# Optimization experiments

Hardware: AMD Instinct MI355X
Metric: run time of the kernel (lower is better)

## Reference

```python
import jax, jax.numpy as jnp
import numpy as np

GEN_POLY = ("1011011", "1111001")  # constraint_length 7, rate 1/2
LARGE = 1e9  # metric for infeasible start states


def _build_trellis(gen_poly):
    """Static trellis tables (numpy, built at trace time).

    State = last mu input bits (most recent bit is MSB), matching the
    shift-register convention: next_state = [u, s_bits[:-1]].
    """
    conv_n = len(gen_poly)
    K = len(gen_poly[0])
    mu = K - 1
    ns, ni, no = 2 ** mu, 2, 2 ** conv_n
    g = np.array([[int(c) for c in p] for p in gen_poly])  # (conv_n, K)
    to_nodes = np.zeros((ns, ni), np.int32)
    op = np.zeros((ns, ni), np.int32)
    for s in range(ns):
        s_bits = [(s >> (mu - 1 - i)) & 1 for i in range(mu)]
        for u in range(ni):
            reg = np.array([u] + s_bits)          # [u_t, u_{t-1}, ..., u_{t-mu}]
            outs = (g @ reg) % 2                  # conv_n output bits
            op[s, u] = int("".join(map(str, outs)), 2)
            to_nodes[s, u] = int("".join(map(str, [u] + s_bits[:-1])), 2)
    from_nodes = np.zeros((ns, ni), np.int32)
    op_by_tonode = np.zeros((ns, ni), np.int32)
    cnt = np.zeros(ns, np.int32)
    for s in range(ns):
        for u in range(ni):
            t = to_nodes[s, u]
            from_nodes[t, cnt[t]] = s
            op_by_tonode[t, cnt[t]] = op[s, u]
            cnt[t] += 1
    op_bits = np.array([[(o >> (conv_n - 1 - j)) & 1 for j in range(conv_n)]
                        for o in range(no)], np.float32)  # (no, conv_n)
    return conv_n, ns, ni, to_nodes, from_nodes, op_by_tonode, op_bits


def setup_inputs() -> dict:
    key = jax.random.key(0)
    # noisy channel LLRs for B=512 codewords of length n=4096
    inputs = jax.random.normal(key, (512, 4096), dtype=jnp.float32) * 2.0
    return {"inputs": inputs}


def reference(inputs):
    conv_n, ns, ni, to_nodes_np, from_nodes_np, op_by_tonode_np, op_bits = \
        _build_trellis(GEN_POLY)
    tn = jnp.asarray(to_nodes_np)       # (ns, ni) next state
    fn = jnp.asarray(from_nodes_np)     # (ns, ni) predecessor states
    opt = jnp.asarray(op_by_tonode_np)  # (ns, ni) output symbol on that branch

    B, n = inputs.shape
    T = n // conv_n                     # number of trellis steps / info bits
    y = inputs.reshape(B, T, conv_n)

    # soft_llr branch metrics: bm[t,b,o] = sum_c y[b,t,c] * (1 - 2*op_bit[o,c])
    sign = jnp.asarray(1.0 - 2.0 * op_bits)          # (no, conv_n)
    bm = jnp.einsum('btc,oc->tbo', y, sign)          # (T, B, no)

    cum0 = jnp.full((B, ns), LARGE, jnp.float32).at[:, 0].set(0.0)
    st_rng = jnp.arange(ns)

    def acs(cum, bm_t):
        # add: metric of (prev_state i, output symbol j)
        sm = bm_t[:, None, :] + cum[:, :, None]      # (B, ns, no)
        # gather by to-node: candidates for each next state
        cand = sm[:, fn, opt]                        # (B, ns, ni)
        j = jnp.argmin(cand, axis=2)                 # compare-select
        tb = fn[st_rng[None, :], j]                  # traceback predecessor (B, ns)
        cum_t = jnp.min(cand, axis=2)
        return cum_t, (cum_t, tb)

    cum_T, (cms, tbs) = jax.lax.scan(acs, cum0, bm)  # tbs: (T, B, ns)

    # traceback from optimal terminal state
    term = jnp.argmin(cum_T, axis=1).astype(jnp.int32)

    def tb_step(st, tb_t):
        prev = jnp.take_along_axis(tb_t, st[:, None], axis=1)[:, 0]
        return prev, st

    p0, ys = jax.lax.scan(tb_step, term, tbs[1:], reverse=True)
    # path states at times 0..T (initial state is 0)
    paths = jnp.concatenate(
        [jnp.zeros((B, 1), jnp.int32), p0[:, None], jnp.swapaxes(ys, 0, 1)],
        axis=1)                                       # (B, T+1)

    # recover input bit per transition: bit u s.t. to_nodes[prev, u] == next
    match = tn[paths[:, :-1]] == paths[:, 1:][:, :, None]  # (B, T, ni)
    bits = jnp.sum(jnp.where(match, jnp.arange(ni, dtype=jnp.int32), 0), axis=-1)
    return bits.astype(jnp.float32)                   # (B, T) hard bit estimates
```

## Files before the change

### kernel.cpp

```cpp
#include <hip/hip_runtime.h>
#include <stdint.h>

#define T_STEPS 2048
#define NCHUNK  86
#define LARGEF  1.0e9f
#define NB      512
typedef unsigned long long u64;
typedef unsigned uint2v __attribute__((ext_vector_type(2)));

__device__ __forceinline__ int par6(int x) { return __builtin_popcount((unsigned)x) & 1; }

constexpr int CARR[6] = {5, 6, 12, 8, 16, 32};

template<int CTRL>
__device__ __forceinline__ float xdpp(float x) {
  return __int_as_float(__builtin_amdgcn_update_dpp(0, __float_as_int(x), CTRL, 0xF, 0xF, true));
}
template<int CTRL>
__device__ __forceinline__ unsigned xdpp_u(unsigned x) {
  return (unsigned)__builtin_amdgcn_update_dpp(0, (int)x, CTRL, 0xF, 0xF, true);
}
__device__ __forceinline__ unsigned selmask_u(unsigned a_false, unsigned b_true, u64 m) {
  unsigned out;
  asm("v_cndmask_b32 %0, %1, %2, %3" : "=v"(out) : "v"(a_false), "v"(b_true), "s"(m));
  return out;
}
__device__ __forceinline__ unsigned exch16_u(unsigned x, u64 mrx) {
#if __has_builtin(__builtin_amdgcn_permlane16_swap)
  uint2v r = __builtin_amdgcn_permlane16_swap(x, x, false, false);
  return selmask_u(r.y, r.x, mrx);
#else
  (void)mrx;
  return (unsigned)__builtin_amdgcn_ds_swizzle((int)x, 0x401F);
#endif
}
__device__ __forceinline__ unsigned exch32_u(unsigned x, u64 mrx) {
#if __has_builtin(__builtin_amdgcn_permlane32_swap)
  uint2v r = __builtin_amdgcn_permlane32_swap(x, x, false, false);
  return selmask_u(r.y, r.x, mrx);
#else
  (void)mrx;
  return (unsigned)__shfl_xor((int)x, 32, 64);
#endif
}
template<int PH>
__device__ __forceinline__ float exchf(float x, const u64 (&mrx)[2]) {
  if constexpr (PH == 0) return xdpp<0xB1>(x);
  else if constexpr (PH == 1) return xdpp<0x4E>(x);
  else if constexpr (PH == 2) return xdpp<0x141>(x);
  else if constexpr (PH == 3) return xdpp<0x140>(x);
  else if constexpr (PH == 4) return __uint_as_float(exch16_u(__float_as_uint(x), mrx[0]));
  else return __uint_as_float(exch32_u(__float_as_uint(x), mrx[1]));
}
template<int PH>
__device__ __forceinline__ unsigned exchu(unsigned x, const u64 (&mrx)[2]) {
  if constexpr (PH == 0) return xdpp_u<0xB1>(x);
  else if constexpr (PH == 1) return xdpp_u<0x4E>(x);
  else if constexpr (PH == 2) return xdpp_u<0x141>(x);
  else if constexpr (PH == 3) return xdpp_u<0x140>(x);
  else if constexpr (PH == 4) return exch16_u(x, mrx[0]);
  else return exch32_u(x, mrx[1]);
}

struct Phc {
  float sae[6], sbe[6];
  unsigned sgn[6];
  unsigned pdu[6];
  u64 pdm[6];
  u64 mrx[2];
};

__device__ __forceinline__ void mkconsts(int lane, Phc& p) {
#pragma unroll
  for (int ph = 0; ph < 6; ++ph) {
    const int pdv = par6(lane & CARR[ph]);
    int t = 0;
#pragma unroll
    for (int j = 0; j < 5; ++j) t |= par6(lane & CARR[(ph + 1 + j) % 6]) << j;
    t |= pdv << 5;
    const float sa = 1.0f - 2.0f * (float)par6(t & 45);
    const float sb = 1.0f - 2.0f * (float)par6(t & 60);
    p.sae[ph] = pdv ? -sa : sa;
    p.sbe[ph] = pdv ? -sb : sb;
    p.sgn[ph] = pdv ? 0u : 0x80000000u;
    p.pdu[ph] = (unsigned)pdv;
    p.pdm[ph] = __ballot(pdv != 0);
  }
  const u64 ODD16 = 0xFFFF0000FFFF0000ull, HI32 = 0xFFFFFFFF00000000ull;
#if __has_builtin(__builtin_amdgcn_permlane16_swap)
  {
    uint2v r = __builtin_amdgcn_permlane16_swap((unsigned)lane, (unsigned)lane, false, false);
    p.mrx[0] = (((unsigned)__builtin_amdgcn_readlane((int)r.x, 0) == 16u)) ? ~ODD16 : ODD16;
  }
#else
  p.mrx[0] = 0;
#endif
#if __has_builtin(__builtin_amdgcn_permlane32_swap)
  {
    uint2v r = __builtin_amdgcn_permlane32_swap((unsigned)lane, (unsigned)lane, false, false);
    p.mrx[1] = (((unsigned)__builtin_amdgcn_readlane((int)r.x, 0) == 32u)) ? ~HI32 : HI32;
  }
#else
  p.mrx[1] = 0;
#endif
}

template<int N>
__device__ __forceinline__ void bmcalc(const float4 (&fy)[12], float (&bm)[24],
                                       const float (&sae)[6], const float (&sbe)[6]) {
#pragma unroll
  for (int k = 0; k < N; ++k) {
    const int ph = k % 6;
    const float y0 = (k & 1) ? fy[k >> 1].z : fy[k >> 1].x;
    const float y1 = (k & 1) ? fy[k >> 1].w : fy[k >> 1].y;
    bm[k] = fmaf(sae[ph], y0, sbe[ph] * y1);
  }
}

template<int N, int K>
__device__ __forceinline__ void acs(float& cum, unsigned& dw, const float (&bm)[24],
                                    const unsigned (&sgn)[6], const u64 (&mrx)[2]) {
  if constexpr (K < N) {
    constexpr int ph = K % 6;
    const float ex = exchf<ph>(cum, mrx);
    const float cA = cum + bm[K];
    const float cB = ex - bm[K];
    const float D = cA - cB;
    cum = fminf(cA, cB);
    unsigned tmp;
    asm("v_xor_b32 %0, %2, %3\n\t"
        "v_cmp_gt_f32 vcc, 0, %0\n\t"
        "v_addc_co_u32 %1, vcc, %1, %1, vcc"
        : "=&v"(tmp), "+v"(dw)
        : "v"(D), "v"(sgn[ph]) : "vcc");
    acs<N, K + 1>(cum, dw, bm, sgn, mrx);
  }
}

template<int N, int K>
__device__ __forceinline__ void wrec(unsigned& word, unsigned& dws, const unsigned (&pdu)[6],
                                     const u64 (&pdm)[6], const u64 (&mrx)[2]) {
  if constexpr (K < N) {
    constexpr int ph = K % 6;
    const unsigned exw = exchu<ph>(word, mrx);
    asm("v_cmp_gt_i32 vcc, 0, %1\n\t"
        "v_add_u32 %1, %1, %1\n\t"
        "s_xor_b64 vcc, vcc, %3\n\t"
        "v_cndmask_b32 %0, %0, %2, vcc"
        : "+v"(word), "+v"(dws)
        : "v"(exw), "s"(pdm[ph]) : "vcc");
    word |= pdu[ph] << (6 + K);
    wrec<N, K + 1>(word, dws, pdu, pdm, mrx);
  }
}

__device__ __forceinline__ int term_argmin(float cum, int lane) {
  const int stf = par6(lane & 12) | (par6(lane & 8) << 1) | (par6(lane & 16) << 2) |
                  (par6(lane & 32) << 3) | (par6(lane & 5) << 4) | (par6(lane & 6) << 5);
  float v = cum; int bs = stf; int bl = lane;
#pragma unroll
  for (int off = 32; off >= 1; off >>= 1) {
    const float ov = __shfl_xor(v, off, 64);
    const int os = __shfl_xor(bs, off, 64);
    const int ol = __shfl_xor(bl, off, 64);
    if (ov < v || (ov == v && os < bs)) { v = ov; bs = os; bl = ol; }
  }
  return bl;
}

__global__ __launch_bounds__(64, 1) void vit_fwd(const float* __restrict__ in,
                                                 unsigned* __restrict__ dwg,
                                                 int* __restrict__ term) {
  __shared__ float y_lds[2 * T_STEPS];
  const int b = blockIdx.x;
  const int lane = threadIdx.x;
  {
    const float4* g = (const float4*)(in + (size_t)b * (2 * T_STEPS));
    float4* l = (float4*)y_lds;
#pragma unroll
    for (int i = 0; i < 16; ++i) l[i * 64 + lane] = g[i * 64 + lane];
  }
  __syncthreads();

  Phc p;
  mkconsts(lane, p);

  float cum = (lane == 0) ? 0.0f : LARGEF;
  float bm[24];
  float4 cur[12], nxt[12];
  const float4* y4 = (const float4*)y_lds;
  unsigned* dwp = dwg + (size_t)b * (NCHUNK * 64) + lane;
  unsigned dw;
#pragma unroll
  for (int j = 0; j < 12; ++j) cur[j] = y4[j];
  for (int cc = 0; cc < 42; ++cc) {
    const int c0 = 2 * cc;
    bmcalc<24>(cur, bm, p.sae, p.sbe);
#pragma unroll
    for (int j = 0; j < 12; ++j) nxt[j] = y4[12 * (c0 + 1) + j];
    dw = 0; acs<24, 0>(cum, dw, bm, p.sgn, p.mrx);
    *dwp = dw; dwp += 64;
    bmcalc<24>(nxt, bm, p.sae, p.sbe);
#pragma unroll
    for (int j = 0; j < 12; ++j) cur[j] = y4[12 * (c0 + 2) + j];
    dw = 0; acs<24, 0>(cum, dw, bm, p.sgn, p.mrx);
    *dwp = dw; dwp += 64;
  }
  bmcalc<24>(cur, bm, p.sae, p.sbe);
#pragma unroll
  for (int j = 0; j < 4; ++j) nxt[j] = y4[1020 + j];
  dw = 0; acs<24, 0>(cum, dw, bm, p.sgn, p.mrx);
  *dwp = dw; dwp += 64;
  bmcalc<8>(nxt, bm, p.sae, p.sbe);
  dw = 0; acs<8, 0>(cum, dw, bm, p.sgn, p.mrx);
  *dwp = dw;

  const int bl = term_argmin(cum, lane);
  if (lane == 0) term[b] = bl;
}

__global__ __launch_bounds__(256, 1) void vit_rec(const unsigned* __restrict__ dwg,
                                                  unsigned* __restrict__ tbfg) {
  const int tid = threadIdx.x;
  const int lane = tid & 63;
  const int wv = tid >> 6;
  const int idx = blockIdx.x * 4 + wv;
  const unsigned ui = (unsigned)idx;
  const int c = (int)(ui % (unsigned)NCHUNK);

  Phc p;
  mkconsts(lane, p);

  const unsigned dw = dwg[(size_t)idx * 64 + lane];
  unsigned word = (unsigned)lane;
  if (c == NCHUNK - 1) {
    unsigned dws = dw << 24;
    wrec<8, 0>(word, dws, p.pdu, p.pdm, p.mrx);
  } else {
    unsigned dws = dw << 8;
    wrec<24, 0>(word, dws, p.pdu, p.pdm, p.mrx);
  }
  tbfg[(size_t)idx * 64 + lane] = word;
}

__global__ __launch_bounds__(64, 1) void vit_tb(const unsigned* __restrict__ tbfg,
                                                const int* __restrict__ term,
                                                float* __restrict__ out) {
  const int b = blockIdx.x;
  const int lane = threadIdx.x;
  unsigned rows[NCHUNK];
  const unsigned* tp = tbfg + (size_t)b * (NCHUNK * 64) + lane;
#pragma unroll
  for (int c = 0; c < NCHUNK; ++c) rows[c] = tp[c * 64];
  int lam = term[b];
  const size_t ob = (size_t)b * T_STEPS;
#pragma unroll
  for (int cc = 0; cc < NCHUNK; ++cc) {
    const int c = NCHUNK - 1 - cc;
    const unsigned w = (unsigned)__builtin_amdgcn_readlane((int)rows[c], lam);
    const int nb = (c == NCHUNK - 1) ? 8 : 24;
    if (lane < nb) out[ob + c * 24 + lane] = (float)((w >> (6 + lane)) & 1u);
    lam = (int)(w & 63u);
  }
}

__global__ __launch_bounds__(64, 1) void vit_fb(const float* __restrict__ in,
                                                float* __restrict__ out) {
  __shared__ float y_lds[2 * T_STEPS];
  __shared__ unsigned dwl[NCHUNK][64];
  __shared__ unsigned tbf[NCHUNK][64];
  const int b = blockIdx.x;
  const int lane = threadIdx.x;
  {
    const float4* g = (const float4*)(in + (size_t)b * (2 * T_STEPS));
    float4* l = (float4*)y_lds;
#pragma unroll
    for (int i = 0; i < 16; ++i) l[i * 64 + lane] = g[i * 64 + lane];
  }
  __syncthreads();
  Phc p;
  mkconsts(lane, p);
  float cum = (lane == 0) ? 0.0f : LARGEF;
  float bm[24];
  float4 cur[12], nxt[12];
  const float4* y4 = (const float4*)y_lds;
  unsigned dw;
#pragma unroll
  for (int j = 0; j < 12; ++j) cur[j] = y4[j];
  for (int cc = 0; cc < 42; ++cc) {
    const int c0 = 2 * cc;
    bmcalc<24>(cur, bm, p.sae, p.sbe);
#pragma unroll
    for (int j = 0; j < 12; ++j) nxt[j] = y4[12 * (c0 + 1) + j];
    dw = 0; acs<24, 0>(cum, dw, bm, p.sgn, p.mrx);
    dwl[c0][lane] = dw;
    bmcalc<24>(nxt, bm, p.sae, p.sbe);
#pragma unroll
    for (int j = 0; j < 12; ++j) cur[j] = y4[12 * (c0 + 2) + j];
    dw = 0; acs<24, 0>(cum, dw, bm, p.sgn, p.mrx);
    dwl[c0 + 1][lane] = dw;
  }
  bmcalc<24>(cur, bm, p.sae, p.sbe);
#pragma unroll
  for (int j = 0; j < 4; ++j) nxt[j] = y4[1020 + j];
  dw = 0; acs<24, 0>(cum, dw, bm, p.sgn, p.mrx);
  dwl[84][lane] = dw;
  bmcalc<8>(nxt, bm, p.sae, p.sbe);
  dw = 0; acs<8, 0>(cum, dw, bm, p.sgn, p.mrx);
  dwl[85][lane] = dw;

  for (int c = 0; c < 85; ++c) {
    unsigned dws = dwl[c][lane] << 8;
    unsigned word = (unsigned)lane;
    wrec<24, 0>(word, dws, p.pdu, p.pdm, p.mrx);
    tbf[c][lane] = word;
  }
  {
    unsigned dws = dwl[85][lane] << 24;
    unsigned word = (unsigned)lane;
    wrec<8, 0>(word, dws, p.pdu, p.pdm, p.mrx);
    tbf[85][lane] = word;
  }

  int lam = __builtin_amdgcn_readfirstlane(term_argmin(cum, lane));
  const size_t ob = (size_t)b * T_STEPS;
  unsigned row = tbf[85][lane];
  for (int c = 85; c >= 0; --c) {
    unsigned nrow = 0;
    if (c > 0) nrow = tbf[c - 1][lane];
    const unsigned w = (unsigned)__builtin_amdgcn_readlane((int)row, lam);
    const int nb = (c == 85) ? 8 : 24;
    if (lane < nb) out[ob + c * 24 + lane] = (float)((w >> (6 + lane)) & 1u);
    lam = (int)(w & 63u);
    row = nrow;
  }
}

extern "C" void kernel_launch(void* const* d_in, const int* in_sizes, int n_in,
                              void* d_out, int out_size, void* d_ws, size_t ws_size,
                              hipStream_t stream) {
  const float* in = (const float*)d_in[0];
  float* out = (float*)d_out;
  (void)in_sizes; (void)n_in; (void)out_size;
  const size_t nwords = (size_t)NB * NCHUNK * 64;
  const size_t need = nwords * 4 * 2 + NB * 4;
  if (ws_size >= need) {
    unsigned* dwg = (unsigned*)d_ws;
    unsigned* tbfg = dwg + nwords;
    int* term = (int*)(tbfg + nwords);
    vit_fwd<<<dim3(NB), dim3(64), 0, stream>>>(in, dwg, term);
    vit_rec<<<dim3((NB * NCHUNK) / 4), dim3(256), 0, stream>>>(dwg, tbfg);
    vit_tb<<<dim3(NB), dim3(64), 0, stream>>>(tbfg, term, out);
  } else {
    vit_fb<<<dim3(NB), dim3(64), 0, stream>>>(in, out);
  }
}
```

Baseline: 75.94 us.

## Checkpoint path metrics in forward pass and recompute decisions per chunk in parallel

```diff
diff --git a/kernel.cpp b/kernel.cpp
--- a/kernel.cpp
+++ b/kernel.cpp
@@ -7,6 +7,7 @@
 #define NB      512
 typedef unsigned long long u64;
 typedef unsigned uint2v __attribute__((ext_vector_type(2)));
+typedef float f32x2 __attribute__((ext_vector_type(2)));
 
 __device__ __forceinline__ int par6(int x) { return __builtin_popcount((unsigned)x) & 1; }
 
@@ -70,88 +71,48 @@
   u64 mrx[2];
 };
 
+__device__ __forceinline__ void mk_sasb(int lane, int ph, float& sae, float& sbe, int& pdv) {
+  pdv = par6(lane & CARR[ph]);
+  int t = 0;
+#pragma unroll
+  for (int j = 0; j < 5; ++j) t |= par6(lane & CARR[(ph + 1 + j) % 6]) << j;
+  t |= pdv << 5;
+  const float sa = 1.0f - 2.0f * (float)par6(t & 45);
+  const float sb = 1.0f - 2.0f * (float)par6(t & 60);
+  sae = pdv ? -sa : sa;
+  sbe = pdv ? -sb : sb;
+}
+
+__device__ __forceinline__ void mk_mrx(int lane, u64 (&mrx)[2]) {
+  const u64 ODD16 = 0xFFFF0000FFFF0000ull, HI32 = 0xFFFFFFFF00000000ull;
+#if __has_builtin(__builtin_amdgcn_permlane16_swap)
+  {
+    uint2v r = __builtin_amdgcn_permlane16_swap((unsigned)lane, (unsigned)lane, false, false);
+    mrx[0] = (((unsigned)__builtin_amdgcn_readlane((int)r.x, 0) == 16u)) ? ~ODD16 : ODD16;
+  }
+#else
+  mrx[0] = 0;
+#endif
+#if __has_builtin(__builtin_amdgcn_permlane32_swap)
+  {
+    uint2v r = __builtin_amdgcn_permlane32_swap((unsigned)lane, (unsigned)lane, false, false);
+    mrx[1] = (((unsigned)__builtin_amdgcn_readlane((int)r.x, 0) == 32u)) ? ~HI32 : HI32;
+  }
+#else
+  mrx[1] = 0;
+#endif
+}
+
 __device__ __forceinline__ void mkconsts(int lane, Phc& p) {
 #pragma unroll
   for (int ph = 0; ph < 6; ++ph) {
-    const int pdv = par6(lane & CARR[ph]);
-    int t = 0;
-#pragma unroll
-    for (int j = 0; j < 5; ++j) t |= par6(lane & CARR[(ph + 1 + j) % 6]) << j;
-    t |= pdv << 5;
-    const float sa = 1.0f - 2.0f * (float)par6(t & 45);
-    const float sb = 1.0f - 2.0f * (float)par6(t & 60);
-    p.sae[ph] = pdv ? -sa : sa;
-    p.sbe[ph] = pdv ? -sb : sb;
+    int pdv;
+    mk_sasb(lane, ph, p.sae[ph], p.sbe[ph], pdv);
     p.sgn[ph] = pdv ? 0u : 0x80000000u;
     p.pdu[ph] = (unsigned)pdv;
     p.pdm[ph] = __ballot(pdv != 0);
   }
-  const u64 ODD16 = 0xFFFF0000FFFF0000ull, HI32 = 0xFFFFFFFF00000000ull;
-#if __has_builtin(__builtin_amdgcn_permlane16_swap)
-  {
-    uint2v r = __builtin_amdgcn_permlane16_swap((unsigned)lane, (unsigned)lane, false, false);
-    p.mrx[0] = (((unsigned)__builtin_amdgcn_readlane((int)r.x, 0) == 16u)) ? ~ODD16 : ODD16;
-  }
-#else
-  p.mrx[0] = 0;
-#endif
-#if __has_builtin(__builtin_amdgcn_permlane32_swap)
-  {
-    uint2v r = __builtin_amdgcn_permlane32_swap((unsigned)lane, (unsigned)lane, false, false);
-    p.mrx[1] = (((unsigned)__builtin_amdgcn_readlane((int)r.x, 0) == 32u)) ? ~HI32 : HI32;
-  }
-#else
-  p.mrx[1] = 0;
-#endif
-}
-
-template<int N>
-__device__ __forceinline__ void bmcalc(const float4 (&fy)[12], float (&bm)[24],
-                                       const float (&sae)[6], const float (&sbe)[6]) {
-#pragma unroll
-  for (int k = 0; k < N; ++k) {
-    const int ph = k % 6;
-    const float y0 = (k & 1) ? fy[k >> 1].z : fy[k >> 1].x;
-    const float y1 = (k & 1) ? fy[k >> 1].w : fy[k >> 1].y;
-    bm[k] = fmaf(sae[ph], y0, sbe[ph] * y1);
-  }
-}
-
-template<int N, int K>
-__device__ __forceinline__ void acs(float& cum, unsigned& dw, const float (&bm)[24],
-                                    const unsigned (&sgn)[6], const u64 (&mrx)[2]) {
-  if constexpr (K < N) {
-    constexpr int ph = K % 6;
-    const float ex = exchf<ph>(cum, mrx);
-    const float cA = cum + bm[K];
-    const float cB = ex - bm[K];
-    const float D = cA - cB;
-    cum = fminf(cA, cB);
-    unsigned tmp;
-    asm("v_xor_b32 %0, %2, %3\n\t"
-        "v_cmp_gt_f32 vcc, 0, %0\n\t"
-        "v_addc_co_u32 %1, vcc, %1, %1, vcc"
-        : "=&v"(tmp), "+v"(dw)
-        : "v"(D), "v"(sgn[ph]) : "vcc");
-    acs<N, K + 1>(cum, dw, bm, sgn, mrx);
-  }
-}
-
-template<int N, int K>
-__device__ __forceinline__ void wrec(unsigned& word, unsigned& dws, const unsigned (&pdu)[6],
-                                     const u64 (&pdm)[6], const u64 (&mrx)[2]) {
-  if constexpr (K < N) {
-    constexpr int ph = K % 6;
-    const unsigned exw = exchu<ph>(word, mrx);
-    asm("v_cmp_gt_i32 vcc, 0, %1\n\t"
-        "v_add_u32 %1, %1, %1\n\t"
-        "s_xor_b64 vcc, vcc, %3\n\t"
-        "v_cndmask_b32 %0, %0, %2, vcc"
-        : "+v"(word), "+v"(dws)
-        : "v"(exw), "s"(pdm[ph]) : "vcc");
-    word |= pdu[ph] << (6 + K);
-    wrec<N, K + 1>(word, dws, pdu, pdm, mrx);
-  }
+  mk_mrx(lane, p.mrx);
 }
 
 __device__ __forceinline__ int term_argmin(float cum, int lane) {
@@ -168,9 +129,56 @@
   return bl;
 }
 
+template<int N, int K>
+__device__ __forceinline__ void acsk1(f32x2& ce, const float4 (&fy)[12],
+                                      const f32x2 (&saep)[6], const f32x2 (&sbep)[6],
+                                      const u64 (&mrx)[2]) {
+  if constexpr (K < N) {
+    constexpr int ph = K % 6;
+    const float y0 = (K & 1) ? fy[K >> 1].z : fy[K >> 1].x;
+    const float y1 = (K & 1) ? fy[K >> 1].w : fy[K >> 1].y;
+    f32x2 y01; y01.x = y0; y01.y = y1;
+    f32x2 t, bmp, cab;
+    asm("v_pk_mul_f32 %0, %1, %2 op_sel:[0,1] op_sel_hi:[1,1]"
+        : "=v"(t) : "v"(sbep[ph]), "v"(y01));
+    asm("v_pk_fma_f32 %0, %1, %2, %3 op_sel:[0,0,0] op_sel_hi:[1,0,1]"
+        : "=v"(bmp) : "v"(saep[ph]), "v"(y01), "v"(t));
+    if constexpr (ph == 0)      ce.y = xdpp<0xB1>(ce.x);
+    else if constexpr (ph == 1) ce.y = xdpp<0x4E>(ce.x);
+    else if constexpr (ph == 2) ce.y = xdpp<0x141>(ce.x);
+    else if constexpr (ph == 3) ce.y = xdpp<0x140>(ce.x);
+    else if constexpr (ph == 4) ce.y = __uint_as_float(exch16_u(__float_as_uint(ce.x), mrx[0]));
+    else                        ce.y = __uint_as_float(exch32_u(__float_as_uint(ce.x), mrx[1]));
+    asm("v_pk_add_f32 %0, %1, %2" : "=v"(cab) : "v"(ce), "v"(bmp));
+    ce.x = fminf(cab.x, cab.y);
+    acsk1<N, K + 1>(ce, fy, saep, sbep, mrx);
+  }
+}
+
+template<int KB, int N, int K>
+__device__ __forceinline__ void rstep(float& cum, unsigned& word, const float4 (&fy)[4],
+                                      const Phc& p) {
+  if constexpr (K < N) {
+    constexpr int ph = (KB + K) % 6;
+    const float y0 = (K & 1) ? fy[K >> 1].z : fy[K >> 1].x;
+    const float y1 = (K & 1) ? fy[K >> 1].w : fy[K >> 1].y;
+    const float bm = fmaf(p.sae[ph], y0, p.sbe[ph] * y1);
+    const float ex = exchf<ph>(cum, p.mrx);
+    const unsigned exw = exchu<ph>(word, p.mrx);
+    const float cA = cum + bm;
+    const float cB = ex - bm;
+    const float D = cA - cB;
+    cum = fminf(cA, cB);
+    const unsigned w0 = selmask_u(word, exw, p.pdm[ph]);
+    const unsigned w1 = selmask_u(exw, word, p.pdm[ph]);
+    const bool d = __uint_as_float(__float_as_uint(D) ^ p.sgn[ph]) < 0.0f;
+    word = (d ? w1 : w0) | (p.pdu[ph] << (6 + KB + K));
+    rstep<KB, N, K + 1>(cum, word, fy, p);
+  }
+}
+
 __global__ __launch_bounds__(64, 1) void vit_fwd(const float* __restrict__ in,
-                                                 unsigned* __restrict__ dwg,
-                                                 int* __restrict__ term) {
+                                                 float* __restrict__ cp) {
   __shared__ float y_lds[2 * T_STEPS];
   const int b = blockIdx.x;
   const int lane = threadIdx.x;
@@ -182,92 +190,138 @@
   }
   __syncthreads();
 
-  Phc p;
-  mkconsts(lane, p);
-
-  float cum = (lane == 0) ? 0.0f : LARGEF;
-  float bm[24];
+  f32x2 saep[6], sbep[6];
+  u64 mrx[2];
+#pragma unroll
+  for (int ph = 0; ph < 6; ++ph) {
+    float sae, sbe; int pdv;
+    mk_sasb(lane, ph, sae, sbe, pdv);
+    saep[ph].x = sae; saep[ph].y = -sae;
+    sbep[ph].x = sbe; sbep[ph].y = -sbe;
+  }
+  mk_mrx(lane, mrx);
+
+  f32x2 ce; ce.x = (lane == 0) ? 0.0f : LARGEF; ce.y = 0.0f;
   float4 cur[12], nxt[12];
   const float4* y4 = (const float4*)y_lds;
-  unsigned* dwp = dwg + (size_t)b * (NCHUNK * 64) + lane;
-  unsigned dw;
+  float* cpp = cp + (size_t)b * (NCHUNK * 64) + lane;
 #pragma unroll
   for (int j = 0; j < 12; ++j) cur[j] = y4[j];
   for (int cc = 0; cc < 42; ++cc) {
     const int c0 = 2 * cc;
-    bmcalc<24>(cur, bm, p.sae, p.sbe);
 #pragma unroll
     for (int j = 0; j < 12; ++j) nxt[j] = y4[12 * (c0 + 1) + j];
-    dw = 0; acs<24, 0>(cum, dw, bm, p.sgn, p.mrx);
-    *dwp = dw; dwp += 64;
-    bmcalc<24>(nxt, bm, p.sae, p.sbe);
+    acsk1<24, 0>(ce, cur, saep, sbep, mrx);
+    cpp[c0 * 64] = ce.x;
 #pragma unroll
     for (int j = 0; j < 12; ++j) cur[j] = y4[12 * (c0 + 2) + j];
-    dw = 0; acs<24, 0>(cum, dw, bm, p.sgn, p.mrx);
-    *dwp = dw; dwp += 64;
-  }
-  bmcalc<24>(cur, bm, p.sae, p.sbe);
+    acsk1<24, 0>(ce, nxt, saep, sbep, mrx);
+    cpp[(c0 + 1) * 64] = ce.x;
+  }
 #pragma unroll
   for (int j = 0; j < 4; ++j) nxt[j] = y4[1020 + j];
-  dw = 0; acs<24, 0>(cum, dw, bm, p.sgn, p.mrx);
-  *dwp = dw; dwp += 64;
-  bmcalc<8>(nxt, bm, p.sae, p.sbe);
-  dw = 0; acs<8, 0>(cum, dw, bm, p.sgn, p.mrx);
-  *dwp = dw;
-
-  const int bl = term_argmin(cum, lane);
-  if (lane == 0) term[b] = bl;
-}
-
-__global__ __launch_bounds__(256, 1) void vit_rec(const unsigned* __restrict__ dwg,
-                                                  unsigned* __restrict__ tbfg) {
+  acsk1<24, 0>(ce, cur, saep, sbep, mrx);
+  cpp[84 * 64] = ce.x;
+  acsk1<8, 0>(ce, nxt, saep, sbep, mrx);
+  cpp[85 * 64] = ce.x;
+}
+
+__global__ __launch_bounds__(1024, 1) void vit_rc(const float* __restrict__ in,
+                                                  const float* __restrict__ cp,
+                                                  float* __restrict__ out) {
+  __shared__ float y_lds[2 * T_STEPS];
+  __shared__ unsigned tbf[NCHUNK][64];
   const int tid = threadIdx.x;
   const int lane = tid & 63;
   const int wv = tid >> 6;
-  const int idx = blockIdx.x * 4 + wv;
-  const unsigned ui = (unsigned)idx;
-  const int c = (int)(ui % (unsigned)NCHUNK);
-
+  const int b = blockIdx.x;
+  {
+    const float4* g = (const float4*)(in + (size_t)b * (2 * T_STEPS));
+    float4* l = (float4*)y_lds;
+    l[tid] = g[tid];
+  }
   Phc p;
   mkconsts(lane, p);
-
-  const unsigned dw = dwg[(size_t)idx * 64 + lane];
-  unsigned word = (unsigned)lane;
-  if (c == NCHUNK - 1) {
-    unsigned dws = dw << 24;
-    wrec<8, 0>(word, dws, p.pdu, p.pdm, p.mrx);
-  } else {
-    unsigned dws = dw << 8;
-    wrec<24, 0>(word, dws, p.pdu, p.pdm, p.mrx);
-  }
-  tbfg[(size_t)idx * 64 + lane] = word;
-}
-
-__global__ __launch_bounds__(64, 1) void vit_tb(const unsigned* __restrict__ tbfg,
-                                                const int* __restrict__ term,
-                                                float* __restrict__ out) {
-  const int b = blockIdx.x;
-  const int lane = threadIdx.x;
-  unsigned rows[NCHUNK];
-  const unsigned* tp = tbfg + (size_t)b * (NCHUNK * 64) + lane;
-#pragma unroll
-  for (int c = 0; c < NCHUNK; ++c) rows[c] = tp[c * 64];
-  int lam = term[b];
-  const size_t ob = (size_t)b * T_STEPS;
-#pragma unroll
-  for (int cc = 0; cc < NCHUNK; ++cc) {
-    const int c = NCHUNK - 1 - cc;
-    const unsigned w = (unsigned)__builtin_amdgcn_readlane((int)rows[c], lam);
-    const int nb = (c == NCHUNK - 1) ? 8 : 24;
-    if (lane < nb) out[ob + c * 24 + lane] = (float)((w >> (6 + lane)) & 1u);
-    lam = (int)(w & 63u);
-  }
-}
-
+  __syncthreads();
+
+  const int cbeg = wv * 6;
+  if (cbeg < NCHUNK) {
+    const int cend = (cbeg + 6 < NCHUNK) ? cbeg + 6 : NCHUNK;
+    for (int c = cbeg; c < cend; ++c) {
+      float cum = (c == 0) ? ((lane == 0) ? 0.0f : LARGEF)
+                           : cp[(size_t)b * (NCHUNK * 64) + (c - 1) * 64 + lane];
+      unsigned word = (unsigned)lane;
+      const float4* yc = ((const float4*)y_lds) + 12 * c;
+      if (c != NCHUNK - 1) {
+        float4 fy[4];
+#pragma unroll
+        for (int j = 0; j < 4; ++j) fy[j] = yc[j];
+        rstep<0, 8, 0>(cum, word, fy, p);
+#pragma unroll
+        for (int j = 0; j < 4; ++j) fy[j] = yc[4 + j];
+        rstep<8, 8, 0>(cum, word, fy, p);
+#pragma unroll
+        for (int j = 0; j < 4; ++j) fy[j] = yc[8 + j];
+        rstep<16, 8, 0>(cum, word, fy, p);
+      } else {
+        float4 fy[4];
+#pragma unroll
+        for (int j = 0; j < 4; ++j) fy[j] = yc[j];
+        rstep<0, 8, 0>(cum, word, fy, p);
+      }
+      tbf[c][lane] = word;
+    }
+  }
+  __syncthreads();
+
+  if (wv == 0) {
+    const float cumF = cp[(size_t)b * (NCHUNK * 64) + 85 * 64 + lane];
+    int lam = __builtin_amdgcn_readfirstlane(term_argmin(cumF, lane));
+    const size_t ob = (size_t)b * T_STEPS;
+    unsigned row = tbf[NCHUNK - 1][lane];
+    for (int c = NCHUNK - 1; c >= 0; --c) {
+      unsigned nrow = 0;
+      if (c > 0) nrow = tbf[c - 1][lane];
+      const unsigned w = (unsigned)__builtin_amdgcn_readlane((int)row, lam);
+      const int nb = (c == NCHUNK - 1) ? 8 : 24;
+      if (lane < nb) out[ob + c * 24 + lane] = (float)((w >> (6 + lane)) & 1u);
+      lam = (int)(w & 63u);
+      row = nrow;
+    }
+  }
+}
+
+template<int N, int K>
+__device__ __forceinline__ void fb_step(float& cum, unsigned& word, const float (&bm)[24],
+                                        const Phc& p) {
+  if constexpr (K < N) {
+    constexpr int ph = K % 6;
+    const float ex = exchf<ph>(cum, p.mrx);
+    const unsigned exw = exchu<ph>(word, p.mrx);
+    const float cA = cum + bm[K];
+    const float cB = ex - bm[K];
+    const float D = cA - cB;
+    cum = fminf(cA, cB);
+    const unsigned w0 = selmask_u(word, exw, p.pdm[ph]);
+    const unsigned w1 = selmask_u(exw, word, p.pdm[ph]);
+    const bool d = __uint_as_float(__float_as_uint(D) ^ p.sgn[ph]) < 0.0f;
+    word = (d ? w1 : w0) | (p.pdu[ph] << (6 + K));
+    fb_step<N, K + 1>(cum, word, bm, p);
+  }
+}
+template<int N>
+__device__ __forceinline__ void fb_bm(const float4 (&fy)[12], float (&bm)[24], const Phc& p) {
+#pragma unroll
+  for (int k = 0; k < N; ++k) {
+    const int ph = k % 6;
+    const float y0 = (k & 1) ? fy[k >> 1].z : fy[k >> 1].x;
+    const float y1 = (k & 1) ? fy[k >> 1].w : fy[k >> 1].y;
+    bm[k] = fmaf(p.sae[ph], y0, p.sbe[ph] * y1);
+  }
+}
 __global__ __launch_bounds__(64, 1) void vit_fb(const float* __restrict__ in,
                                                 float* __restrict__ out) {
   __shared__ float y_lds[2 * T_STEPS];
-  __shared__ unsigned dwl[NCHUNK][64];
   __shared__ unsigned tbf[NCHUNK][64];
   const int b = blockIdx.x;
   const int lane = threadIdx.x;
@@ -281,46 +335,33 @@
   Phc p;
   mkconsts(lane, p);
   float cum = (lane == 0) ? 0.0f : LARGEF;
+  unsigned word = (unsigned)lane;
   float bm[24];
   float4 cur[12], nxt[12];
   const float4* y4 = (const float4*)y_lds;
-  unsigned dw;
 #pragma unroll
   for (int j = 0; j < 12; ++j) cur[j] = y4[j];
   for (int cc = 0; cc < 42; ++cc) {
     const int c0 = 2 * cc;
-    bmcalc<24>(cur, bm, p.sae, p.sbe);
+    fb_bm<24>(cur, bm, p);
 #pragma unroll
     for (int j = 0; j < 12; ++j) nxt[j] = y4[12 * (c0 + 1) + j];
-    dw = 0; acs<24, 0>(cum, dw, bm, p.sgn, p.mrx);
-    dwl[c0][lane] = dw;
-    bmcalc<24>(nxt, bm, p.sae, p.sbe);
+    fb_step<24, 0>(cum, word, bm, p);
+    tbf[c0][lane] = word; word = (unsigned)lane;
+    fb_bm<24>(nxt, bm, p);
 #pragma unroll
     for (int j = 0; j < 12; ++j) cur[j] = y4[12 * (c0 + 2) + j];
-    dw = 0; acs<24, 0>(cum, dw, bm, p.sgn, p.mrx);
-    dwl[c0 + 1][lane] = dw;
-  }
-  bmcalc<24>(cur, bm, p.sae, p.sbe);
+    fb_step<24, 0>(cum, word, bm, p);
+    tbf[c0 + 1][lane] = word; word = (unsigned)lane;
+  }
+  fb_bm<24>(cur, bm, p);
 #pragma unroll
   for (int j = 0; j < 4; ++j) nxt[j] = y4[1020 + j];
-  dw = 0; acs<24, 0>(cum, dw, bm, p.sgn, p.mrx);
-  dwl[84][lane] = dw;
-  bmcalc<8>(nxt, bm, p.sae, p.sbe);
-  dw = 0; acs<8, 0>(cum, dw, bm, p.sgn, p.mrx);
-  dwl[85][lane] = dw;
-
-  for (int c = 0; c < 85; ++c) {
-    unsigned dws = dwl[c][lane] << 8;
-    unsigned word = (unsigned)lane;
-    wrec<24, 0>(word, dws, p.pdu, p.pdm, p.mrx);
-    tbf[c][lane] = word;
-  }
-  {
-    unsigned dws = dwl[85][lane] << 24;
-    unsigned word = (unsigned)lane;
-    wrec<8, 0>(word, dws, p.pdu, p.pdm, p.mrx);
-    tbf[85][lane] = word;
-  }
+  fb_step<24, 0>(cum, word, bm, p);
+  tbf[84][lane] = word; word = (unsigned)lane;
+  fb_bm<8>(nxt, bm, p);
+  fb_step<8, 0>(cum, word, bm, p);
+  tbf[85][lane] = word;
 
   int lam = __builtin_amdgcn_readfirstlane(term_argmin(cum, lane));
   const size_t ob = (size_t)b * T_STEPS;
@@ -342,15 +383,11 @@
   const float* in = (const float*)d_in[0];
   float* out = (float*)d_out;
   (void)in_sizes; (void)n_in; (void)out_size;
-  const size_t nwords = (size_t)NB * NCHUNK * 64;
-  const size_t need = nwords * 4 * 2 + NB * 4;
+  const size_t need = (size_t)NB * NCHUNK * 64 * 4;
   if (ws_size >= need) {
-    unsigned* dwg = (unsigned*)d_ws;
-    unsigned* tbfg = dwg + nwords;
-    int* term = (int*)(tbfg + nwords);
-    vit_fwd<<<dim3(NB), dim3(64), 0, stream>>>(in, dwg, term);
-    vit_rec<<<dim3((NB * NCHUNK) / 4), dim3(256), 0, stream>>>(dwg, tbfg);
-    vit_tb<<<dim3(NB), dim3(64), 0, stream>>>(tbfg, term, out);
+    float* cp = (float*)d_ws;
+    vit_fwd<<<dim3(NB), dim3(64), 0, stream>>>(in, cp);
+    vit_rc<<<dim3(NB), dim3(1024), 0, stream>>>(in, cp, out);
   } else {
     vit_fb<<<dim3(NB), dim3(64), 0, stream>>>(in, out);
   }
```

New measurement: 90.91 us. 1.2x slower.

## Fuse chunk reconstruction and traceback into one per-codeword kernel via LDS

Applied to the files above, without the earlier changes.

```diff
diff --git a/kernel.cpp b/kernel.cpp
--- a/kernel.cpp
+++ b/kernel.cpp
@@ -70,39 +70,48 @@
   u64 mrx[2];
 };
 
-__device__ __forceinline__ void mkconsts(int lane, Phc& p) {
-#pragma unroll
-  for (int ph = 0; ph < 6; ++ph) {
-    const int pdv = par6(lane & CARR[ph]);
-    int t = 0;
-#pragma unroll
-    for (int j = 0; j < 5; ++j) t |= par6(lane & CARR[(ph + 1 + j) % 6]) << j;
-    t |= pdv << 5;
-    const float sa = 1.0f - 2.0f * (float)par6(t & 45);
-    const float sb = 1.0f - 2.0f * (float)par6(t & 60);
-    p.sae[ph] = pdv ? -sa : sa;
-    p.sbe[ph] = pdv ? -sb : sb;
-    p.sgn[ph] = pdv ? 0u : 0x80000000u;
-    p.pdu[ph] = (unsigned)pdv;
-    p.pdm[ph] = __ballot(pdv != 0);
-  }
+__device__ __forceinline__ void mk_sasb(int lane, int ph, float& sae, float& sbe, int& pdv) {
+  pdv = par6(lane & CARR[ph]);
+  int t = 0;
+#pragma unroll
+  for (int j = 0; j < 5; ++j) t |= par6(lane & CARR[(ph + 1 + j) % 6]) << j;
+  t |= pdv << 5;
+  const float sa = 1.0f - 2.0f * (float)par6(t & 45);
+  const float sb = 1.0f - 2.0f * (float)par6(t & 60);
+  sae = pdv ? -sa : sa;
+  sbe = pdv ? -sb : sb;
+}
+
+__device__ __forceinline__ void mk_mrx(int lane, u64 (&mrx)[2]) {
   const u64 ODD16 = 0xFFFF0000FFFF0000ull, HI32 = 0xFFFFFFFF00000000ull;
 #if __has_builtin(__builtin_amdgcn_permlane16_swap)
   {
     uint2v r = __builtin_amdgcn_permlane16_swap((unsigned)lane, (unsigned)lane, false, false);
-    p.mrx[0] = (((unsigned)__builtin_amdgcn_readlane((int)r.x, 0) == 16u)) ? ~ODD16 : ODD16;
+    mrx[0] = (((unsigned)__builtin_amdgcn_readlane((int)r.x, 0) == 16u)) ? ~ODD16 : ODD16;
   }
 #else
-  p.mrx[0] = 0;
+  mrx[0] = 0;
 #endif
 #if __has_builtin(__builtin_amdgcn_permlane32_swap)
   {
     uint2v r = __builtin_amdgcn_permlane32_swap((unsigned)lane, (unsigned)lane, false, false);
-    p.mrx[1] = (((unsigned)__builtin_amdgcn_readlane((int)r.x, 0) == 32u)) ? ~HI32 : HI32;
+    mrx[1] = (((unsigned)__builtin_amdgcn_readlane((int)r.x, 0) == 32u)) ? ~HI32 : HI32;
   }
 #else
-  p.mrx[1] = 0;
+  mrx[1] = 0;
 #endif
+}
+
+__device__ __forceinline__ void mkconsts(int lane, Phc& p) {
+#pragma unroll
+  for (int ph = 0; ph < 6; ++ph) {
+    int pdv;
+    mk_sasb(lane, ph, p.sae[ph], p.sbe[ph], pdv);
+    p.sgn[ph] = pdv ? 0u : 0x80000000u;
+    p.pdu[ph] = (unsigned)pdv;
+    p.pdm[ph] = __ballot(pdv != 0);
+  }
+  mk_mrx(lane, p.mrx);
 }
 
 template<int N>
@@ -219,55 +228,78 @@
   if (lane == 0) term[b] = bl;
 }
 
-__global__ __launch_bounds__(256, 1) void vit_rec(const unsigned* __restrict__ dwg,
-                                                  unsigned* __restrict__ tbfg) {
+__global__ __launch_bounds__(512, 1) void vit_rc(const unsigned* __restrict__ dwg,
+                                                 const int* __restrict__ term,
+                                                 float* __restrict__ out) {
+  __shared__ unsigned tbf[NCHUNK][64];
   const int tid = threadIdx.x;
   const int lane = tid & 63;
   const int wv = tid >> 6;
-  const int idx = blockIdx.x * 4 + wv;
-  const unsigned ui = (unsigned)idx;
-  const int c = (int)(ui % (unsigned)NCHUNK);
-
-  Phc p;
-  mkconsts(lane, p);
-
-  const unsigned dw = dwg[(size_t)idx * 64 + lane];
-  unsigned word = (unsigned)lane;
-  if (c == NCHUNK - 1) {
-    unsigned dws = dw << 24;
-    wrec<8, 0>(word, dws, p.pdu, p.pdm, p.mrx);
-  } else {
-    unsigned dws = dw << 8;
-    wrec<24, 0>(word, dws, p.pdu, p.pdm, p.mrx);
-  }
-  tbfg[(size_t)idx * 64 + lane] = word;
-}
-
-__global__ __launch_bounds__(64, 1) void vit_tb(const unsigned* __restrict__ tbfg,
-                                                const int* __restrict__ term,
-                                                float* __restrict__ out) {
   const int b = blockIdx.x;
-  const int lane = threadIdx.x;
-  unsigned rows[NCHUNK];
-  const unsigned* tp = tbfg + (size_t)b * (NCHUNK * 64) + lane;
-#pragma unroll
-  for (int c = 0; c < NCHUNK; ++c) rows[c] = tp[c * 64];
-  int lam = term[b];
-  const size_t ob = (size_t)b * T_STEPS;
-#pragma unroll
-  for (int cc = 0; cc < NCHUNK; ++cc) {
-    const int c = NCHUNK - 1 - cc;
-    const unsigned w = (unsigned)__builtin_amdgcn_readlane((int)rows[c], lam);
-    const int nb = (c == NCHUNK - 1) ? 8 : 24;
-    if (lane < nb) out[ob + c * 24 + lane] = (float)((w >> (6 + lane)) & 1u);
-    lam = (int)(w & 63u);
-  }
-}
-
+
+  unsigned pdu[6];
+  u64 pdm[6], mrx[2];
+#pragma unroll
+  for (int ph = 0; ph < 6; ++ph) {
+    const int pdv = par6(lane & CARR[ph]);
+    pdu[ph] = (unsigned)pdv;
+    pdm[ph] = __ballot(pdv != 0);
+  }
+  mk_mrx(lane, mrx);
+
+  const int cbeg = wv * 11;
+  const int cend = (cbeg + 11 < NCHUNK) ? cbeg + 11 : NCHUNK;
+  for (int c = cbeg; c < cend; ++c) {
+    const unsigned dw = dwg[((size_t)b * NCHUNK + c) * 64 + lane];
+    unsigned word = (unsigned)lane;
+    if (c == NCHUNK - 1) {
+      unsigned dws = dw << 24;
+      wrec<8, 0>(word, dws, pdu, pdm, mrx);
+    } else {
+      unsigned dws = dw << 8;
+      wrec<24, 0>(word, dws, pdu, pdm, mrx);
+    }
+    tbf[c][lane] = word;
+  }
+  __syncthreads();
+
+  if (wv == 0) {
+    int lam = __builtin_amdgcn_readfirstlane(term[b]);
+    const size_t ob = (size_t)b * T_STEPS;
+    unsigned row = tbf[NCHUNK - 1][lane];
+    for (int c = NCHUNK - 1; c >= 0; --c) {
+      unsigned nrow = 0;
+      if (c > 0) nrow = tbf[c - 1][lane];
+      const unsigned w = (unsigned)__builtin_amdgcn_readlane((int)row, lam);
+      const int nb = (c == NCHUNK - 1) ? 8 : 24;
+      if (lane < nb) out[ob + c * 24 + lane] = (float)((w >> (6 + lane)) & 1u);
+      lam = (int)(w & 63u);
+      row = nrow;
+    }
+  }
+}
+
+template<int N, int K>
+__device__ __forceinline__ void fb_step(float& cum, unsigned& word, const float (&bm)[24],
+                                        const Phc& p) {
+  if constexpr (K < N) {
+    constexpr int ph = K % 6;
+    const float ex = exchf<ph>(cum, p.mrx);
+    const unsigned exw = exchu<ph>(word, p.mrx);
+    const float cA = cum + bm[K];
+    const float cB = ex - bm[K];
+    const float D = cA - cB;
+    cum = fminf(cA, cB);
+    const unsigned w0 = selmask_u(word, exw, p.pdm[ph]);
+    const unsigned w1 = selmask_u(exw, word, p.pdm[ph]);
+    const bool d = __uint_as_float(__float_as_uint(D) ^ p.sgn[ph]) < 0.0f;
+    word = (d ? w1 : w0) | (p.pdu[ph] << (6 + K));
+    fb_step<N, K + 1>(cum, word, bm, p);
+  }
+}
 __global__ __launch_bounds__(64, 1) void vit_fb(const float* __restrict__ in,
                                                 float* __restrict__ out) {
   __shared__ float y_lds[2 * T_STEPS];
-  __shared__ unsigned dwl[NCHUNK][64];
   __shared__ unsigned tbf[NCHUNK][64];
   const int b = blockIdx.x;
   const int lane = threadIdx.x;
@@ -281,10 +313,10 @@
   Phc p;
   mkconsts(lane, p);
   float cum = (lane == 0) ? 0.0f : LARGEF;
+  unsigned word = (unsigned)lane;
   float bm[24];
   float4 cur[12], nxt[12];
   const float4* y4 = (const float4*)y_lds;
-  unsigned dw;
 #pragma unroll
   for (int j = 0; j < 12; ++j) cur[j] = y4[j];
   for (int cc = 0; cc < 42; ++cc) {
@@ -292,35 +324,22 @@
     bmcalc<24>(cur, bm, p.sae, p.sbe);
 #pragma unroll
     for (int j = 0; j < 12; ++j) nxt[j] = y4[12 * (c0 + 1) + j];
-    dw = 0; acs<24, 0>(cum, dw, bm, p.sgn, p.mrx);
-    dwl[c0][lane] = dw;
+    fb_step<24, 0>(cum, word, bm, p);
+    tbf[c0][lane] = word; word = (unsigned)lane;
     bmcalc<24>(nxt, bm, p.sae, p.sbe);
 #pragma unroll
     for (int j = 0; j < 12; ++j) cur[j] = y4[12 * (c0 + 2) + j];
-    dw = 0; acs<24, 0>(cum, dw, bm, p.sgn, p.mrx);
-    dwl[c0 + 1][lane] = dw;
+    fb_step<24, 0>(cum, word, bm, p);
+    tbf[c0 + 1][lane] = word; word = (unsigned)lane;
   }
   bmcalc<24>(cur, bm, p.sae, p.sbe);
 #pragma unroll
   for (int j = 0; j < 4; ++j) nxt[j] = y4[1020 + j];
-  dw = 0; acs<24, 0>(cum, dw, bm, p.sgn, p.mrx);
-  dwl[84][lane] = dw;
+  fb_step<24, 0>(cum, word, bm, p);
+  tbf[84][lane] = word; word = (unsigned)lane;
   bmcalc<8>(nxt, bm, p.sae, p.sbe);
-  dw = 0; acs<8, 0>(cum, dw, bm, p.sgn, p.mrx);
-  dwl[85][lane] = dw;
-
-  for (int c = 0; c < 85; ++c) {
-    unsigned dws = dwl[c][lane] << 8;
-    unsigned word = (unsigned)lane;
-    wrec<24, 0>(word, dws, p.pdu, p.pdm, p.mrx);
-    tbf[c][lane] = word;
-  }
-  {
-    unsigned dws = dwl[85][lane] << 24;
-    unsigned word = (unsigned)lane;
-    wrec<8, 0>(word, dws, p.pdu, p.pdm, p.mrx);
-    tbf[85][lane] = word;
-  }
+  fb_step<8, 0>(cum, word, bm, p);
+  tbf[85][lane] = word;
 
   int lam = __builtin_amdgcn_readfirstlane(term_argmin(cum, lane));
   const size_t ob = (size_t)b * T_STEPS;
@@ -343,14 +362,12 @@
   float* out = (float*)d_out;
   (void)in_sizes; (void)n_in; (void)out_size;
   const size_t nwords = (size_t)NB * NCHUNK * 64;
-  const size_t need = nwords * 4 * 2 + NB * 4;
+  const size_t need = nwords * 4 + NB * 4;
   if (ws_size >= need) {
     unsigned* dwg = (unsigned*)d_ws;
-    unsigned* tbfg = dwg + nwords;
-    int* term = (int*)(tbfg + nwords);
+    int* term = (int*)(dwg + nwords);
     vit_fwd<<<dim3(NB), dim3(64), 0, stream>>>(in, dwg, term);
-    vit_rec<<<dim3((NB * NCHUNK) / 4), dim3(256), 0, stream>>>(dwg, tbfg);
-    vit_tb<<<dim3(NB), dim3(64), 0, stream>>>(tbfg, term, out);
+    vit_rc<<<dim3(NB), dim3(512), 0, stream>>>(dwg, term, out);
   } else {
     vit_fb<<<dim3(NB), dim3(64), 0, stream>>>(in, out);
   }
```

After: 70.20 us. -7.6%, faster.
